# Optimization experiments

Hardware: AMD Instinct MI355X
Metric: run time of the kernel (lower is better)

The kernel has to match this reference:

```python
import jax, jax.numpy as jnp
import numpy as np
import math

B, Z, D = 1024, 32768, 128

def setup_inputs() -> dict:
    key = jax.random.key(0)
    k1, k2, k3 = jax.random.split(key, 3)
    z_sparse = jax.random.randint(k1, (B, Z), 0, 2, dtype=jnp.int32)
    context_embedding = jax.random.normal(k2, (B, D), dtype=jnp.float32)
    embd_table = jax.random.normal(k3, (Z, D), dtype=jnp.float32)  # nn.Embedding weight
    return {"z_sparse": z_sparse, "context_embedding": context_embedding, "embd_table": embd_table}

def reference(z_sparse, context_embedding, embd_table):
    # mask[b, z] = feature z active in batch b  (matches (z_sparse > 0).nonzero())
    mask = z_sparse > 0  # [B, Z]
    # attn_scores = (ctx * emb).sum(-1) / sqrt(D), densified over all (b, z)
    scores = (context_embedding @ embd_table.T) / math.sqrt(embd_table.shape[1])  # [B, Z]
    # per-batch softmax over active features only
    masked = jnp.where(mask, scores, -jnp.inf)
    w = jax.nn.softmax(masked, axis=-1)
    w = jnp.where(mask, w, 0.0)  # zero inactive (also kills NaN for all-empty rows)
    # scatter-add of emb * weight == weighted matmul against the table
    out = w @ embd_table  # [B, D]
    counts = jnp.clip(jnp.sum(mask, axis=-1), 1, None)  # bincount(...).clamp(min=1)
    return out / counts[:, None].astype(out.dtype)
```

## Files before the change

kernel.cpp:

```cpp
#include <hip/hip_runtime.h>
#include <stdint.h>

#define B_SZ 1024
#define Z_SZ 32768
#define D_SZ 128
#define NZ   64
#define CZ   (Z_SZ / NZ)
#define TZ   64
#define ITERS (CZ / TZ)
#define TBLK 128
#define NWAVE 4
#define WROWS 32

#define SEMB_STRIDE  136
#define SEMBT_STRIDE 72
#define ST_STRIDE    136

#define NB_TAB  (Z_SZ / 64)

#define WS_O   0
#define WS_M   (NZ * B_SZ * D_SZ)
#define WS_L   (WS_M + NZ * B_SZ)
#define WS_C   (WS_L + NZ * B_SZ)
#define WS_TAB (WS_C + NZ * B_SZ)

typedef short bf16x8  __attribute__((ext_vector_type(8)));
typedef float f32x4   __attribute__((ext_vector_type(4)));
typedef float f32x16  __attribute__((ext_vector_type(16)));

#if __has_builtin(__builtin_amdgcn_exp2f)
#define EXP2F(x) __builtin_amdgcn_exp2f(x)
#else
#define EXP2F(x) exp2f(x)
#endif

__device__ __forceinline__ unsigned short f2bf(float f) {
    union { float f; uint32_t u; } v; v.f = f;
    uint32_t u = v.u;
    u = (u + 0x7FFFu + ((u >> 16) & 1u)) >> 16;
    return (unsigned short)u;
}
__device__ __forceinline__ uint32_t packbf(float a, float b) {
    return (uint32_t)f2bf(a) | ((uint32_t)f2bf(b) << 16);
}

__global__ __launch_bounds__(256) void prep(
    const float*    __restrict__ emb,
    unsigned short* __restrict__ embR,
    unsigned short* __restrict__ embT)
{
    __shared__ __align__(16) unsigned short st[64 * ST_STRIDE];
    const int z0 = blockIdx.x * 64;
    const int t  = threadIdx.x;
    {
        const int r = t >> 2, q = t & 3;
        const float* src = emb + (size_t)(z0 + r) * D_SZ + q * 32;
        unsigned short* dR = embR + (size_t)(z0 + r) * D_SZ + q * 32;
        unsigned short* dL = st + r * ST_STRIDE + q * 32;
#pragma unroll
        for (int u = 0; u < 8; ++u) {
            float4 x = *(const float4*)(src + 4 * u);
            ushort4 h;
            h.x = f2bf(x.x); h.y = f2bf(x.y); h.z = f2bf(x.z); h.w = f2bf(x.w);
            *(ushort4*)(dR + 4 * u) = h;
            *(ushort4*)(dL + 4 * u) = h;
        }
    }
    __syncthreads();
    {
        const int lane = t & 63, w = t >> 6;
#pragma unroll
        for (int i = 0; i < 4; ++i) {
            const int d = w * 32 + i * 8 + (lane >> 3);
            const int c = lane & 7;
            bf16x8 v;
#pragma unroll
            for (int k = 0; k < 8; ++k) v[k] = (short)st[(c * 8 + k) * ST_STRIDE + d];
            *(bf16x8*)(embT + (size_t)d * Z_SZ + z0 + c * 8) = v;
        }
    }
}

__global__ __launch_bounds__(256, 2) void attn_part(
    const int*            __restrict__ zs,
    const float*          __restrict__ ctx,
    const unsigned short* __restrict__ embR,
    const unsigned short* __restrict__ embT,
    float*                __restrict__ ws)
{
    __shared__ __align__(16) unsigned short s_embA [2][TZ   * SEMB_STRIDE];
    __shared__ __align__(16) unsigned short s_embTA[2][D_SZ * SEMBT_STRIDE];

    const int tid  = threadIdx.x;
    const int lane = tid & 63;
    const int l31  = lane & 31;
    const int hi   = lane >> 5;

    const int bg     = blockIdx.x;
    const int ch     = blockIdx.y;
    const int z_base = ch * CZ;
    const int wb0    = bg * TBLK + (tid >> 6) * WROWS;
    const int brow   = wb0 + l31;

    const int srow = tid >> 2, sq3 = tid & 3;
    const int sd   = tid >> 1, sh  = tid & 1;

    const int* zrow = zs + (size_t)brow * Z_SZ + hi * 4;

    bf16x8 afrag[8];
    {
        const float scale = (float)(1.4426950408889634 * 0.08838834764831845);
        const float* crow = ctx + (size_t)brow * D_SZ;
#pragma unroll
        for (int ks = 0; ks < 8; ++ks) {
            const float* p = crow + ks * 16 + hi * 8;
            float4 x0 = *(const float4*)(p);
            float4 x1 = *(const float4*)(p + 4);
            bf16x8 a;
            a[0] = (short)f2bf(x0.x * scale); a[1] = (short)f2bf(x0.y * scale);
            a[2] = (short)f2bf(x0.z * scale); a[3] = (short)f2bf(x0.w * scale);
            a[4] = (short)f2bf(x1.x * scale); a[5] = (short)f2bf(x1.y * scale);
            a[6] = (short)f2bf(x1.z * scale); a[7] = (short)f2bf(x1.w * scale);
            afrag[ks] = a;
        }
    }

    float m_s = -1e30f, l_s = 0.f;
    int   cnt = 0;
    f32x16 acc[4];
#pragma unroll
    for (int n = 0; n < 4; ++n)
#pragma unroll
        for (int e = 0; e < 16; ++e) acc[n][e] = 0.f;

    bf16x8 rA[4], rT[4];
    int4   mc[2][4], mn[2][4];

    {
        const unsigned short* srcR = embR + (size_t)(z_base + srow) * D_SZ + sq3 * 32;
        const unsigned short* srcT = embT + (size_t)sd * Z_SZ + z_base + sh * 32;
#pragma unroll
        for (int u = 0; u < 4; ++u) { rA[u] = *(const bf16x8*)(srcR + u * 8); }
#pragma unroll
        for (int u = 0; u < 4; ++u) { rT[u] = *(const bf16x8*)(srcT + u * 8); }
#pragma unroll
        for (int nt = 0; nt < 2; ++nt)
#pragma unroll
            for (int g = 0; g < 4; ++g)
                mc[nt][g] = *(const int4*)(zrow + z_base + nt * 32 + g * 8);
    }
    {
        unsigned short* dA = s_embA[0] + srow * SEMB_STRIDE + sq3 * 32;
        unsigned short* dT = s_embTA[0] + sd * SEMBT_STRIDE + sh * 32;
#pragma unroll
        for (int u = 0; u < 4; ++u) *(bf16x8*)(dA + u * 8) = rA[u];
#pragma unroll
        for (int u = 0; u < 4; ++u) *(bf16x8*)(dT + u * 8) = rT[u];
    }
    if (ITERS > 1) {
        const int z1 = z_base + TZ;
        const unsigned short* srcR = embR + (size_t)(z1 + srow) * D_SZ + sq3 * 32;
        const unsigned short* srcT = embT + (size_t)sd * Z_SZ + z1 + sh * 32;
#pragma unroll
        for (int u = 0; u < 4; ++u) { rA[u] = *(const bf16x8*)(srcR + u * 8); }
#pragma unroll
        for (int u = 0; u < 4; ++u) { rT[u] = *(const bf16x8*)(srcT + u * 8); }
    }

    int cur = 0;
    for (int it = 0; it < ITERS; ++it) {
        __syncthreads();

        if (it + 1 < ITERS) {
            const int z0n = z_base + (it + 1) * TZ;
#pragma unroll
            for (int nt = 0; nt < 2; ++nt)
#pragma unroll
                for (int g = 0; g < 4; ++g)
                    mn[nt][g] = *(const int4*)(zrow + z0n + nt * 32 + g * 8);
        }

        const unsigned short* se = s_embA[cur];
        const unsigned short* st_ = s_embTA[cur];

        f32x16 sfr[2];
#pragma unroll
        for (int nt = 0; nt < 2; ++nt) {
            f32x16 c;
#pragma unroll
            for (int e = 0; e < 16; ++e) c[e] = 0.f;
            const unsigned short* bb = se + (nt * 32 + l31) * SEMB_STRIDE + hi * 8;
#pragma unroll
            for (int ks = 0; ks < 8; ++ks) {
                bf16x8 ef = *(const bf16x8*)(bb + ks * 16);
                c = __builtin_amdgcn_mfma_f32_32x32x16_bf16(ef, afrag[ks], c, 0, 0, 0);
            }
            sfr[nt] = c;
        }

        int bit[2][16];
#pragma unroll
        for (int nt = 0; nt < 2; ++nt) {
#pragma unroll
            for (int g = 0; g < 4; ++g) {
                bit[nt][4*g+0] = (mc[nt][g].x > 0) ? 1 : 0;
                bit[nt][4*g+1] = (mc[nt][g].y > 0) ? 1 : 0;
                bit[nt][4*g+2] = (mc[nt][g].z > 0) ? 1 : 0;
                bit[nt][4*g+3] = (mc[nt][g].w > 0) ? 1 : 0;
                cnt += bit[nt][4*g+0] + bit[nt][4*g+1] + bit[nt][4*g+2] + bit[nt][4*g+3];
            }
        }

        float tm = -1e30f;
#pragma unroll
        for (int nt = 0; nt < 2; ++nt) {
#pragma unroll
            for (int r = 0; r < 16; r += 4) {
                float a0 = bit[nt][r+0] ? sfr[nt][r+0] : -1e30f;
                float a1 = bit[nt][r+1] ? sfr[nt][r+1] : -1e30f;
                float a2 = bit[nt][r+2] ? sfr[nt][r+2] : -1e30f;
                float a3 = bit[nt][r+3] ? sfr[nt][r+3] : -1e30f;
                tm = fmaxf(tm, fmaxf(fmaxf(a0, a1), fmaxf(a2, a3)));
            }
        }
        tm = fmaxf(tm, __shfl_xor(tm, 32));

        if (__any(tm > m_s + 8.f)) {
            float mnew = fmaxf(m_s, tm);
            float al = EXP2F(m_s - mnew);
            m_s = mnew;
            l_s *= al;
#pragma unroll
            for (int n = 0; n < 4; ++n)
#pragma unroll
                for (int e = 0; e < 16; ++e) acc[n][e] *= al;
        }

        uint32_t q[8][2];
        float ps = 0.f;
#pragma unroll
        for (int nt = 0; nt < 2; ++nt) {
#pragma unroll
            for (int g = 0; g < 4; ++g) {
                float p0 = bit[nt][4*g+0] ? EXP2F(sfr[nt][4*g+0] - m_s) : 0.f;
                float p1 = bit[nt][4*g+1] ? EXP2F(sfr[nt][4*g+1] - m_s) : 0.f;
                float p2 = bit[nt][4*g+2] ? EXP2F(sfr[nt][4*g+2] - m_s) : 0.f;
                float p3 = bit[nt][4*g+3] ? EXP2F(sfr[nt][4*g+3] - m_s) : 0.f;
                ps += (p0 + p1) + (p2 + p3);
                q[4*nt+g][0] = packbf(p0, p1);
                q[4*nt+g][1] = packbf(p2, p3);
            }
        }
        ps += __shfl_xor(ps, 32);
        l_s += ps;

        bf16x8 pfrag[4];
#pragma unroll
        for (int ks2 = 0; ks2 < 4; ++ks2) {
            uint32_t s0 = hi ? q[2*ks2][0] : q[2*ks2+1][0];
            uint32_t s1 = hi ? q[2*ks2][1] : q[2*ks2+1][1];
            uint32_t r0 = (uint32_t)__shfl_xor((int)s0, 32);
            uint32_t r1 = (uint32_t)__shfl_xor((int)s1, 32);
            union { uint32_t u[4]; bf16x8 v; } P;
            P.u[0] = hi ? r0 : q[2*ks2][0];
            P.u[1] = hi ? r1 : q[2*ks2][1];
            P.u[2] = hi ? q[2*ks2+1][0] : r0;
            P.u[3] = hi ? q[2*ks2+1][1] : r1;
            pfrag[ks2] = P.v;
        }

#pragma unroll
        for (int nt2 = 0; nt2 < 4; ++nt2) {
            const unsigned short* tb = st_ + (nt2 * 32 + l31) * SEMBT_STRIDE + hi * 8;
#pragma unroll
            for (int ks2 = 0; ks2 < 4; ++ks2) {
                bf16x8 ta = *(const bf16x8*)(tb + ks2 * 16);
                acc[nt2] = __builtin_amdgcn_mfma_f32_32x32x16_bf16(ta, pfrag[ks2], acc[nt2], 0, 0, 0);
            }
        }

        if (it + 1 < ITERS) {
            unsigned short* dA = s_embA[cur ^ 1] + srow * SEMB_STRIDE + sq3 * 32;
            unsigned short* dT = s_embTA[cur ^ 1] + sd * SEMBT_STRIDE + sh * 32;
#pragma unroll
            for (int u = 0; u < 4; ++u) *(bf16x8*)(dA + u * 8) = rA[u];
#pragma unroll
            for (int u = 0; u < 4; ++u) *(bf16x8*)(dT + u * 8) = rT[u];
            if (it + 2 < ITERS) {
                const int z2 = z_base + (it + 2) * TZ;
                const unsigned short* srcR = embR + (size_t)(z2 + srow) * D_SZ + sq3 * 32;
                const unsigned short* srcT = embT + (size_t)sd * Z_SZ + z2 + sh * 32;
#pragma unroll
                for (int u = 0; u < 4; ++u) { rA[u] = *(const bf16x8*)(srcR + u * 8); }
#pragma unroll
                for (int u = 0; u < 4; ++u) { rT[u] = *(const bf16x8*)(srcT + u * 8); }
            }
        }

#pragma unroll
        for (int nt = 0; nt < 2; ++nt)
#pragma unroll
            for (int g = 0; g < 4; ++g) mc[nt][g] = mn[nt][g];
        cur ^= 1;
    }

    {
        float* orow = ws + WS_O + ((size_t)ch * B_SZ + brow) * D_SZ;
#pragma unroll
        for (int nt2 = 0; nt2 < 4; ++nt2) {
#pragma unroll
            for (int g = 0; g < 4; ++g) {
                f32x4 v;
                v[0] = acc[nt2][4*g+0]; v[1] = acc[nt2][4*g+1];
                v[2] = acc[nt2][4*g+2]; v[3] = acc[nt2][4*g+3];
                *(f32x4*)(orow + nt2 * 32 + g * 8 + hi * 4) = v;
            }
        }
    }
    cnt += __shfl_xor(cnt, 32);
    if (lane < 32) {
        ws[WS_M + ch * B_SZ + brow] = m_s;
        ws[WS_L + ch * B_SZ + brow] = l_s;
        ws[WS_C + ch * B_SZ + brow] = (float)cnt;
    }
}

__global__ __launch_bounds__(128) void attn_reduce(
    const float* __restrict__ ws, float* __restrict__ out)
{
    const int b = blockIdx.x;
    const int d = threadIdx.x;
    const float* mP = ws + WS_M;
    const float* lP = ws + WS_L;
    const float* cP = ws + WS_C;

    float M = -1e30f;
#pragma unroll
    for (int c = 0; c < NZ; ++c) M = fmaxf(M, mP[c * B_SZ + b]);

    float L = 0.f, C = 0.f, acc = 0.f;
#pragma unroll
    for (int c = 0; c < NZ; ++c) {
        float w = EXP2F(mP[c * B_SZ + b] - M);
        L += lP[c * B_SZ + b] * w;
        C += cP[c * B_SZ + b];
        acc += ws[WS_O + ((size_t)c * B_SZ + b) * D_SZ + d] * w;
    }
    float cntv = fmaxf(C, 1.0f);
    out[(size_t)b * D_SZ + d] = (L > 0.f) ? acc / (L * cntv) : 0.f;
}

extern "C" void kernel_launch(void* const* d_in, const int* in_sizes, int n_in,
                              void* d_out, int out_size, void* d_ws, size_t ws_size,
                              hipStream_t stream) {
    (void)in_sizes; (void)n_in; (void)out_size; (void)ws_size;
    const int*   zs  = (const int*)  d_in[0];
    const float* ctx = (const float*)d_in[1];
    const float* emb = (const float*)d_in[2];
    float* out = (float*)d_out;
    float* ws  = (float*)d_ws;

    unsigned short* embR = (unsigned short*)(ws + WS_TAB);
    unsigned short* embT = embR + (size_t)Z_SZ * D_SZ;

    prep<<<NB_TAB, 256, 0, stream>>>(emb, embR, embT);

    dim3 grid1(B_SZ / TBLK, NZ);
    attn_part<<<grid1, 256, 0, stream>>>(zs, ctx, embR, embT, ws);
    attn_reduce<<<B_SZ, 128, 0, stream>>>(ws, out);
}
```

Before: 236.8 us.

## Stage partial outputs through LDS for coalesced stores and remap block order

Measured after the change: 242.9 us. +2.6%, slower.

```diff
diff --git a/kernel.cpp b/kernel.cpp
--- a/kernel.cpp
+++ b/kernel.cpp
@@ -15,6 +15,11 @@
 #define SEMB_STRIDE  136
 #define SEMBT_STRIDE 72
 #define ST_STRIDE    136
+#define SO_STRIDE    132
+
+#define ASZ (TZ * SEMB_STRIDE)
+#define TSZ (D_SZ * SEMBT_STRIDE)
+#define ALL_SZ (2 * ASZ + 2 * TSZ)
 
 #define NB_TAB  (Z_SZ / 64)
 
@@ -88,16 +93,16 @@
     const unsigned short* __restrict__ embT,
     float*                __restrict__ ws)
 {
-    __shared__ __align__(16) unsigned short s_embA [2][TZ   * SEMB_STRIDE];
-    __shared__ __align__(16) unsigned short s_embTA[2][D_SZ * SEMBT_STRIDE];
+    __shared__ __align__(16) unsigned short s_all[ALL_SZ];
 
     const int tid  = threadIdx.x;
     const int lane = tid & 63;
     const int l31  = lane & 31;
     const int hi   = lane >> 5;
 
-    const int bg     = blockIdx.x;
-    const int ch     = blockIdx.y;
+    const int lid = blockIdx.y * 8 + blockIdx.x;
+    const int ch  = lid & 63;
+    const int bg  = lid >> 6;
     const int z_base = ch * CZ;
     const int wb0    = bg * TBLK + (tid >> 6) * WROWS;
     const int brow   = wb0 + l31;
@@ -150,8 +155,8 @@
                 mc[nt][g] = *(const int4*)(zrow + z_base + nt * 32 + g * 8);
     }
     {
-        unsigned short* dA = s_embA[0] + srow * SEMB_STRIDE + sq3 * 32;
-        unsigned short* dT = s_embTA[0] + sd * SEMBT_STRIDE + sh * 32;
+        unsigned short* dA = s_all + srow * SEMB_STRIDE + sq3 * 32;
+        unsigned short* dT = s_all + 2 * ASZ + sd * SEMBT_STRIDE + sh * 32;
 #pragma unroll
         for (int u = 0; u < 4; ++u) *(bf16x8*)(dA + u * 8) = rA[u];
 #pragma unroll
@@ -180,8 +185,8 @@
                     mn[nt][g] = *(const int4*)(zrow + z0n + nt * 32 + g * 8);
         }
 
-        const unsigned short* se = s_embA[cur];
-        const unsigned short* st_ = s_embTA[cur];
+        const unsigned short* se  = s_all + cur * ASZ;
+        const unsigned short* st_ = s_all + 2 * ASZ + cur * TSZ;
 
         f32x16 sfr[2];
 #pragma unroll
@@ -280,8 +285,8 @@
         }
 
         if (it + 1 < ITERS) {
-            unsigned short* dA = s_embA[cur ^ 1] + srow * SEMB_STRIDE + sq3 * 32;
-            unsigned short* dT = s_embTA[cur ^ 1] + sd * SEMBT_STRIDE + sh * 32;
+            unsigned short* dA = s_all + (cur ^ 1) * ASZ + srow * SEMB_STRIDE + sq3 * 32;
+            unsigned short* dT = s_all + 2 * ASZ + (cur ^ 1) * TSZ + sd * SEMBT_STRIDE + sh * 32;
 #pragma unroll
             for (int u = 0; u < 4; ++u) *(bf16x8*)(dA + u * 8) = rA[u];
 #pragma unroll
@@ -304,8 +309,10 @@
         cur ^= 1;
     }
 
-    {
-        float* orow = ws + WS_O + ((size_t)ch * B_SZ + brow) * D_SZ;
+    __syncthreads();
+    {
+        float* fs = (float*)s_all;
+        const int rl = (tid >> 6) * WROWS + l31;
 #pragma unroll
         for (int nt2 = 0; nt2 < 4; ++nt2) {
 #pragma unroll
@@ -313,9 +320,19 @@
                 f32x4 v;
                 v[0] = acc[nt2][4*g+0]; v[1] = acc[nt2][4*g+1];
                 v[2] = acc[nt2][4*g+2]; v[3] = acc[nt2][4*g+3];
-                *(f32x4*)(orow + nt2 * 32 + g * 8 + hi * 4) = v;
-            }
-        }
+                *(f32x4*)(fs + rl * SO_STRIDE + nt2 * 32 + g * 8 + hi * 4) = v;
+            }
+        }
+    }
+    __syncthreads();
+    {
+        const float* fs = (const float*)s_all;
+        const int row = tid >> 1, half = tid & 1;
+        const float* src = fs + row * SO_STRIDE + half * 64;
+        float* dst = ws + WS_O + ((size_t)ch * B_SZ + bg * TBLK + row) * D_SZ + half * 64;
+#pragma unroll
+        for (int u = 0; u < 16; ++u)
+            *(f32x4*)(dst + u * 4) = *(const f32x4*)(src + u * 4);
     }
     cnt += __shfl_xor(cnt, 32);
     if (lane < 32) {
```
